# Kernel tuning notes

Measured on AMD Instinct MI355X. Metric: run time of the kernel, lower is better.

## Reference

```python
import jax, jax.numpy as jnp
import numpy as np

B, S, E = 8, 2048, 512
H = 8          # attention heads (and also number of sampling points)
P = 8          # deformable sampling points per token
Dh = E // H


def setup_inputs() -> dict:
    key = jax.random.key(0)
    ks = jax.random.split(key, 9)
    scale = 0.02
    return {
        "q": jax.random.normal(ks[0], (B, S, E), jnp.float32),
        "k": jax.random.normal(ks[1], (B, S, E), jnp.float32),
        "v": jax.random.normal(ks[2], (B, S, E), jnp.float32),
        "offset_w": jax.random.normal(ks[3], (2 * P, E), jnp.float32) * scale,
        "offset_b": jnp.zeros((2 * P,), jnp.float32),
        "in_proj_w": jax.random.normal(ks[4], (3 * E, E), jnp.float32) * scale,
        "in_proj_b": jnp.zeros((3 * E,), jnp.float32),
        "out_w": jax.random.normal(ks[5], (E, E), jnp.float32) * scale,
        "out_b": jnp.zeros((E,), jnp.float32),
    }


def reference(q, k, v, offset_w, offset_b, in_proj_w, in_proj_b, out_w, out_b):
    b, s, e = q.shape
    # learned offsets: [B,S,P,2]; only component 0 is used as a temporal offset
    offsets = (q @ offset_w.T + offset_b).reshape(b, s, P, 2)
    t = jnp.arange(s, dtype=q.dtype)[None, :, None]                # [1,S,1]
    # index = clamp(int(t + off0), 0, S-1); python int() truncates toward zero
    idx = jnp.clip(jnp.trunc(t + offsets[..., 0]).astype(jnp.int32), 0, s - 1)  # [B,S,P]
    # gather sampled K/V: [B,S,P,E]
    sk = jnp.take_along_axis(k[:, :, None, :], idx[..., None], axis=1)
    sv = jnp.take_along_axis(v[:, :, None, :], idx[..., None], axis=1)

    # nn.MultiheadAttention with query len 1 per token, kv len P, batch = B*S
    wq, wk, wv = in_proj_w[:e], in_proj_w[e:2 * e], in_proj_w[2 * e:]
    bq, bk, bv = in_proj_b[:e], in_proj_b[e:2 * e], in_proj_b[2 * e:]
    n = b * s
    qp = (q.reshape(n, e) @ wq.T + bq).reshape(n, H, Dh)            # [N,H,Dh]
    kp = (sk.reshape(n, P, e) @ wk.T + bk).reshape(n, P, H, Dh)     # [N,P,H,Dh]
    vp = (sv.reshape(n, P, e) @ wv.T + bv).reshape(n, P, H, Dh)
    scores = jnp.einsum('nhd,nphd->nhp', qp, kp) / np.sqrt(Dh)      # [N,H,P]
    attn = jax.nn.softmax(scores, axis=-1)
    ctx = jnp.einsum('nhp,nphd->nhd', attn, vp).reshape(n, e)       # [N,E]
    out = ctx @ out_w.T + out_b
    return out.reshape(b, s, e)
```

## Files before the change

kernel.cpp:

```cpp
#include <hip/hip_runtime.h>

#define S_LEN 2048
#define E_DIM 512
#define NTOK  16384

typedef __bf16 bf16x8_t __attribute__((ext_vector_type(8)));
typedef float f32x4_t __attribute__((ext_vector_type(4)));
typedef unsigned short u16x8_t __attribute__((ext_vector_type(8)));

__device__ __forceinline__ float bf2f(unsigned short h) {
  return __uint_as_float(((unsigned)h) << 16);
}
__device__ __forceinline__ u16x8_t cvt8n(float4 a, float4 b) {
  bf16x8_t t;
  t[0] = (__bf16)a.x; t[1] = (__bf16)a.y; t[2] = (__bf16)a.z; t[3] = (__bf16)a.w;
  t[4] = (__bf16)b.x; t[5] = (__bf16)b.y; t[6] = (__bf16)b.z; t[7] = (__bf16)b.w;
  union { bf16x8_t h; u16x8_t u; } cv; cv.h = t; return cv.u;
}
__device__ __forceinline__ void gload16(const void* g, void* l) {
  __builtin_amdgcn_global_load_lds(
      (const __attribute__((address_space(1))) unsigned int*)g,
      (__attribute__((address_space(3))) unsigned int*)l, 16, 0, 0);
}

__global__ __launch_bounds__(256)
void offsets_kernel(const float* __restrict__ q, const float* __restrict__ ow,
                    const float* __restrict__ ob, int* __restrict__ idx,
                    unsigned short* __restrict__ Qbf)
{
  const int wid  = threadIdx.x >> 6;
  const int lane = threadIdx.x & 63;
  const int n = blockIdx.x * 4 + wid;
  const int s = n & (S_LEN - 1);
  const float* qr = q + (size_t)n * E_DIM + lane * 8;
  const float4 q0 = *(const float4*)qr;
  const float4 q1 = *(const float4*)(qr + 4);
  *(u16x8_t*)(Qbf + (size_t)n * E_DIM + lane * 8) = cvt8n(q0, q1);
  float myoff = 0.f;
  #pragma unroll
  for (int p = 0; p < 8; ++p) {
    const float* wr = ow + (size_t)(2 * p) * E_DIM + lane * 8;
    const float4 w0 = *(const float4*)wr;
    const float4 w1 = *(const float4*)(wr + 4);
    float acc = q0.x*w0.x + q0.y*w0.y + q0.z*w0.z + q0.w*w0.w
              + q1.x*w1.x + q1.y*w1.y + q1.z*w1.z + q1.w*w1.w;
    #pragma unroll
    for (int d = 32; d; d >>= 1) acc += __shfl_xor(acc, d, 64);
    if ((lane & 7) == p) myoff = acc;
  }
  if (lane < 8) {
    float off = myoff + ob[2 * lane];
    float val = (float)s + off;
    int id = (int)truncf(val);
    id = id < 0 ? 0 : (id > S_LEN - 1 ? S_LEN - 1 : id);
    idx[n * 8 + lane] = id;
  }
}

__global__ __launch_bounds__(256)
void cvt_kernel(const float* __restrict__ k, const float* __restrict__ v,
                const float* __restrict__ ipw, const float* __restrict__ ow,
                unsigned short* __restrict__ Kb, unsigned short* __restrict__ Vb,
                unsigned short* __restrict__ Wb, unsigned short* __restrict__ OWb)
{
  const int bid = blockIdx.x;
  const float* src; unsigned short* dst; size_t off;
  if (bid < 4096)       { src = k;   dst = Kb;  off = (size_t)bid * 2048; }
  else if (bid < 8192)  { src = v;   dst = Vb;  off = (size_t)(bid - 4096) * 2048; }
  else if (bid < 8576)  { src = ipw; dst = Wb;  off = (size_t)(bid - 8192) * 2048; }
  else                  { src = ow;  dst = OWb; off = (size_t)(bid - 8576) * 2048; }
  const size_t i = off + (size_t)threadIdx.x * 8;
  const float4 a = *(const float4*)(src + i);
  const float4 b = *(const float4*)(src + i + 4);
  *(u16x8_t*)(dst + i) = cvt8n(a, b);
}

template<int OUT_BF16>
__global__ __launch_bounds__(256, 2)
void gemm_kernel(const unsigned short* __restrict__ A0, const unsigned short* __restrict__ A1,
                 const unsigned short* __restrict__ A2, const unsigned short* __restrict__ W,
                 const float* __restrict__ bias, void* __restrict__ Cout)
{
  __shared__ __align__(16) unsigned short sA[2][128 * 64];
  __shared__ __align__(16) unsigned short sB[2][128 * 64];

  const int z = blockIdx.z;
  const unsigned short* A = (z == 0) ? A0 : ((z == 1) ? A1 : A2);
  const unsigned short* Wz = W + (size_t)z * E_DIM * E_DIM;
  const float* bz = bias + (size_t)z * E_DIM;

  const int t    = threadIdx.x;
  const int lane = t & 63;
  const int wid  = t >> 6;
  const int wm   = wid >> 1;
  const int wn   = wid & 1;
  const size_t m0 = (size_t)blockIdx.x * 128;
  const size_t n0 = (size_t)blockIdx.y * 128;

  const int srow0  = wid * 32;
  const int schunk = (lane & 7) ^ (lane >> 3);
  const unsigned short* gA = A  + (m0 + srow0 + (lane >> 3)) * E_DIM + schunk * 8;
  const unsigned short* gB = Wz + (n0 + srow0 + (lane >> 3)) * E_DIM + schunk * 8;

#define STAGE(buf, k0) do { \
    _Pragma("unroll") \
    for (int i_ = 0; i_ < 4; ++i_) { \
      gload16(gA + (size_t)(i_ * 8) * E_DIM + (k0), &sA[buf][(srow0 + i_ * 8) * 64]); \
      gload16(gB + (size_t)(i_ * 8) * E_DIM + (k0), &sB[buf][(srow0 + i_ * 8) * 64]); \
    } } while (0)

  f32x4_t acc[4][4];
  #pragma unroll
  for (int i = 0; i < 4; ++i)
    #pragma unroll
    for (int j = 0; j < 4; ++j)
      acc[i][j] = (f32x4_t){0.f, 0.f, 0.f, 0.f};

  STAGE(0, 0);
  int cur = 0;
  const int fr = lane & 15;
  const int ck0 = lane >> 4;

  for (int kt = 0; kt < 8; ++kt) {
    __syncthreads();
    if (kt < 7) STAGE(cur ^ 1, (kt + 1) * 64);
    #pragma unroll
    for (int kk = 0; kk < 64; kk += 32) {
      const int ckb = (kk >> 3) + ck0;
      bf16x8_t af[4], bfv[4];
      #pragma unroll
      for (int i = 0; i < 4; ++i) {
        const int ra = wm * 64 + i * 16 + fr;
        af[i] = *(const bf16x8_t*)&sA[cur][ra * 64 + ((ckb ^ (ra & 7)) << 3)];
      }
      #pragma unroll
      for (int j = 0; j < 4; ++j) {
        const int rb = wn * 64 + j * 16 + fr;
        bfv[j] = *(const bf16x8_t*)&sB[cur][rb * 64 + ((ckb ^ (rb & 7)) << 3)];
      }
      #pragma unroll
      for (int i = 0; i < 4; ++i)
        #pragma unroll
        for (int j = 0; j < 4; ++j)
          acc[i][j] = __builtin_amdgcn_mfma_f32_16x16x32_bf16(af[i], bfv[j], acc[i][j], 0, 0, 0);
    }
    cur ^= 1;
  }
#undef STAGE

  unsigned short* Cb = (unsigned short*)Cout + (size_t)z * NTOK * E_DIM;
  float* Cf = (float*)Cout;
  #pragma unroll
  for (int i = 0; i < 4; ++i) {
    const int row = (int)m0 + wm * 64 + i * 16 + (lane >> 4) * 4;
    #pragma unroll
    for (int j = 0; j < 4; ++j) {
      const int col = (int)n0 + wn * 64 + j * 16 + fr;
      const float bv = bz[col];
      #pragma unroll
      for (int r = 0; r < 4; ++r) {
        const float val = acc[i][j][r] + bv;
        if constexpr (OUT_BF16)
          Cb[(size_t)(row + r) * E_DIM + col] = __builtin_bit_cast(unsigned short, (__bf16)val);
        else
          Cf[(size_t)(row + r) * E_DIM + col] = val;
      }
    }
  }
}

__global__ __launch_bounds__(256)
void attn_kernel(const unsigned short* __restrict__ Qp, const unsigned short* __restrict__ Kp,
                 const unsigned short* __restrict__ Vp, const int* __restrict__ idx,
                 unsigned short* __restrict__ ctx)
{
  const int wid  = threadIdx.x >> 6;
  const int lane = threadIdx.x & 63;
  const int n = blockIdx.x * 4 + wid;
  const int b = n >> 11;
  const int h = lane >> 3;
  const int p = lane & 7;

  const int id = idx[n * 8 + p];
  const size_t krow = ((size_t)(b << 11) + id) * E_DIM + h * 64;
  const unsigned short* qb = Qp + (size_t)n * E_DIM + h * 64;

  float sc = 0.f;
  #pragma unroll
  for (int j = 0; j < 8; ++j) {
    u16x8_t qv = *(const u16x8_t*)(qb + j * 8);
    u16x8_t kv = *(const u16x8_t*)(Kp + krow + j * 8);
    #pragma unroll
    for (int e = 0; e < 8; ++e) sc += bf2f(qv[e]) * bf2f(kv[e]);
  }
  sc *= 0.125f;

  float m = sc;
  m = fmaxf(m, __shfl_xor(m, 1, 64));
  m = fmaxf(m, __shfl_xor(m, 2, 64));
  m = fmaxf(m, __shfl_xor(m, 4, 64));
  const float ex = __expf(sc - m);
  float dsum = ex;
  dsum += __shfl_xor(dsum, 1, 64);
  dsum += __shfl_xor(dsum, 2, 64);
  dsum += __shfl_xor(dsum, 4, 64);
  const float attn = ex / dsum;

  const int d0 = p * 8;
  float cacc[8];
  #pragma unroll
  for (int j = 0; j < 8; ++j) cacc[j] = 0.f;
  #pragma unroll
  for (int pp = 0; pp < 8; ++pp) {
    const float ap = __shfl(attn, (lane & 56) + pp, 64);
    const int  idp = __shfl(id,   (lane & 56) + pp, 64);
    const unsigned short* vb = Vp + ((size_t)(b << 11) + idp) * E_DIM + h * 64 + d0;
    u16x8_t vv = *(const u16x8_t*)vb;
    #pragma unroll
    for (int j = 0; j < 8; ++j) cacc[j] += ap * bf2f(vv[j]);
  }
  u16x8_t cc;
  #pragma unroll
  for (int j = 0; j < 8; ++j) cc[j] = __builtin_bit_cast(unsigned short, (__bf16)cacc[j]);
  *(u16x8_t*)(ctx + (size_t)n * E_DIM + h * 64 + d0) = cc;
}

extern "C" void kernel_launch(void* const* d_in, const int* in_sizes, int n_in,
                              void* d_out, int out_size, void* d_ws, size_t ws_size,
                              hipStream_t stream) {
  const float* q        = (const float*)d_in[0];
  const float* k        = (const float*)d_in[1];
  const float* v        = (const float*)d_in[2];
  const float* offset_w = (const float*)d_in[3];
  const float* offset_b = (const float*)d_in[4];
  const float* in_proj_w = (const float*)d_in[5];
  const float* in_proj_b = (const float*)d_in[6];
  const float* out_w    = (const float*)d_in[7];
  const float* out_b    = (const float*)d_in[8];

  char* ws = (char*)d_ws;
  unsigned short* Qbf = (unsigned short*)ws;
  unsigned short* Kbf = Qbf + (size_t)NTOK * E_DIM;
  unsigned short* Vbf = Kbf + (size_t)NTOK * E_DIM;
  unsigned short* Wb  = Vbf + (size_t)NTOK * E_DIM;
  unsigned short* OWb = Wb + (size_t)3 * E_DIM * E_DIM;
  unsigned short* Qp  = OWb + (size_t)E_DIM * E_DIM;
  unsigned short* Kp  = Qp + (size_t)NTOK * E_DIM;
  unsigned short* Vp  = Kp + (size_t)NTOK * E_DIM;
  int* idxb = (int*)(Vp + (size_t)NTOK * E_DIM);
  unsigned short* ctxb = Qbf;

  offsets_kernel<<<NTOK / 4, 256, 0, stream>>>(q, offset_w, offset_b, idxb, Qbf);
  cvt_kernel<<<8704, 256, 0, stream>>>(k, v, in_proj_w, out_w, Kbf, Vbf, Wb, OWb);
  gemm_kernel<1><<<dim3(NTOK / 128, E_DIM / 128, 3), 256, 0, stream>>>(
      Qbf, Kbf, Vbf, Wb, in_proj_b, (void*)Qp);
  attn_kernel<<<NTOK / 4, 256, 0, stream>>>(Qp, Kp, Vp, idxb, ctxb);
  gemm_kernel<0><<<dim3(NTOK / 128, E_DIM / 128, 1), 256, 0, stream>>>(
      ctxb, ctxb, ctxb, OWb, out_b, d_out);
}
```

Before: 105.5 us.

## Merge prepass kernels and deepen GEMM pipeline to four-stage K=32 ring

Fuses the offsets and conversion kernels into one launch with block-range dispatch, which removes one kernel launch and its tail. The GEMM moves from a double-buffered K=64 tile to a four-slot ring of K=32 tiles. It uses explicit vmcnt waits, raw barriers and setprio around the MFMA block, so more global loads stay in flight. In exchange it adds two barriers per K-step, a new swizzle and hand-tuned waitcnt counts that could break if the compiler reorders loads.

```diff
diff --git a/kernel.cpp b/kernel.cpp
--- a/kernel.cpp
+++ b/kernel.cpp
@@ -24,13 +24,30 @@
 }
 
 __global__ __launch_bounds__(256)
-void offsets_kernel(const float* __restrict__ q, const float* __restrict__ ow,
+void prepass_kernel(const float* __restrict__ q, const float* __restrict__ k,
+                    const float* __restrict__ v, const float* __restrict__ ipw,
+                    const float* __restrict__ outw, const float* __restrict__ ow,
                     const float* __restrict__ ob, int* __restrict__ idx,
-                    unsigned short* __restrict__ Qbf)
+                    unsigned short* __restrict__ Qbf, unsigned short* __restrict__ Kb,
+                    unsigned short* __restrict__ Vb, unsigned short* __restrict__ Wb,
+                    unsigned short* __restrict__ OWb)
 {
+  const int bid = blockIdx.x;
+  if (bid >= 4096) {
+    const float* src; unsigned short* dst; size_t off;
+    if (bid < 8192)       { src = k;    dst = Kb;  off = (size_t)(bid - 4096) * 2048; }
+    else if (bid < 12288) { src = v;    dst = Vb;  off = (size_t)(bid - 8192) * 2048; }
+    else if (bid < 12672) { src = ipw;  dst = Wb;  off = (size_t)(bid - 12288) * 2048; }
+    else                  { src = outw; dst = OWb; off = (size_t)(bid - 12672) * 2048; }
+    const size_t i = off + (size_t)threadIdx.x * 8;
+    const float4 a = *(const float4*)(src + i);
+    const float4 b = *(const float4*)(src + i + 4);
+    *(u16x8_t*)(dst + i) = cvt8n(a, b);
+    return;
+  }
   const int wid  = threadIdx.x >> 6;
   const int lane = threadIdx.x & 63;
-  const int n = blockIdx.x * 4 + wid;
+  const int n = bid * 4 + wid;
   const int s = n & (S_LEN - 1);
   const float* qr = q + (size_t)n * E_DIM + lane * 8;
   const float4 q0 = *(const float4*)qr;
@@ -57,32 +74,14 @@
   }
 }
 
-__global__ __launch_bounds__(256)
-void cvt_kernel(const float* __restrict__ k, const float* __restrict__ v,
-                const float* __restrict__ ipw, const float* __restrict__ ow,
-                unsigned short* __restrict__ Kb, unsigned short* __restrict__ Vb,
-                unsigned short* __restrict__ Wb, unsigned short* __restrict__ OWb)
-{
-  const int bid = blockIdx.x;
-  const float* src; unsigned short* dst; size_t off;
-  if (bid < 4096)       { src = k;   dst = Kb;  off = (size_t)bid * 2048; }
-  else if (bid < 8192)  { src = v;   dst = Vb;  off = (size_t)(bid - 4096) * 2048; }
-  else if (bid < 8576)  { src = ipw; dst = Wb;  off = (size_t)(bid - 8192) * 2048; }
-  else                  { src = ow;  dst = OWb; off = (size_t)(bid - 8576) * 2048; }
-  const size_t i = off + (size_t)threadIdx.x * 8;
-  const float4 a = *(const float4*)(src + i);
-  const float4 b = *(const float4*)(src + i + 4);
-  *(u16x8_t*)(dst + i) = cvt8n(a, b);
-}
-
 template<int OUT_BF16>
 __global__ __launch_bounds__(256, 2)
 void gemm_kernel(const unsigned short* __restrict__ A0, const unsigned short* __restrict__ A1,
                  const unsigned short* __restrict__ A2, const unsigned short* __restrict__ W,
                  const float* __restrict__ bias, void* __restrict__ Cout)
 {
-  __shared__ __align__(16) unsigned short sA[2][128 * 64];
-  __shared__ __align__(16) unsigned short sB[2][128 * 64];
+  __shared__ __align__(16) unsigned short sA[4][128 * 32];
+  __shared__ __align__(16) unsigned short sB[4][128 * 32];
 
   const int z = blockIdx.z;
   const unsigned short* A = (z == 0) ? A0 : ((z == 1) ? A1 : A2);
@@ -97,17 +96,17 @@
   const size_t m0 = (size_t)blockIdx.x * 128;
   const size_t n0 = (size_t)blockIdx.y * 128;
 
-  const int srow0  = wid * 32;
-  const int schunk = (lane & 7) ^ (lane >> 3);
-  const unsigned short* gA = A  + (m0 + srow0 + (lane >> 3)) * E_DIM + schunk * 8;
-  const unsigned short* gB = Wz + (n0 + srow0 + (lane >> 3)) * E_DIM + schunk * 8;
-
-#define STAGE(buf, k0) do { \
-    _Pragma("unroll") \
-    for (int i_ = 0; i_ < 4; ++i_) { \
-      gload16(gA + (size_t)(i_ * 8) * E_DIM + (k0), &sA[buf][(srow0 + i_ * 8) * 64]); \
-      gload16(gB + (size_t)(i_ * 8) * E_DIM + (k0), &sB[buf][(srow0 + i_ * 8) * 64]); \
-    } } while (0)
+  const int srow   = wid * 32 + (lane >> 2);
+  const int schunk = (lane & 3) ^ ((lane >> 3) & 3);
+  const unsigned short* gA = A  + (m0 + srow) * E_DIM + schunk * 8;
+  const unsigned short* gB = Wz + (n0 + srow) * E_DIM + schunk * 8;
+
+#define STAGE(slot, t_) do { \
+    gload16(gA + (t_) * 32,              &sA[slot][(wid * 32) * 32]); \
+    gload16(gA + (t_) * 32 + 16 * E_DIM, &sA[slot][(wid * 32 + 16) * 32]); \
+    gload16(gB + (t_) * 32,              &sB[slot][(wid * 32) * 32]); \
+    gload16(gB + (t_) * 32 + 16 * E_DIM, &sB[slot][(wid * 32 + 16) * 32]); \
+  } while (0)
 
   f32x4_t acc[4][4];
   #pragma unroll
@@ -116,35 +115,39 @@
     for (int j = 0; j < 4; ++j)
       acc[i][j] = (f32x4_t){0.f, 0.f, 0.f, 0.f};
 
-  STAGE(0, 0);
-  int cur = 0;
-  const int fr = lane & 15;
-  const int ck0 = lane >> 4;
-
-  for (int kt = 0; kt < 8; ++kt) {
-    __syncthreads();
-    if (kt < 7) STAGE(cur ^ 1, (kt + 1) * 64);
-    #pragma unroll
-    for (int kk = 0; kk < 64; kk += 32) {
-      const int ckb = (kk >> 3) + ck0;
-      bf16x8_t af[4], bfv[4];
+  STAGE(0, 0); STAGE(1, 1); STAGE(2, 2);
+
+  const int fr    = lane & 15;
+  const int cswz8 = (((lane >> 4) ^ ((fr >> 1) & 3)) << 3);
+
+  #pragma unroll
+  for (int tt = 0; tt < 16; ++tt) {
+    if (tt + 3 < 16) STAGE((tt + 3) & 3, tt + 3);
+    if (tt < 13)       asm volatile("s_waitcnt vmcnt(12)" ::: "memory");
+    else if (tt == 13) asm volatile("s_waitcnt vmcnt(8)"  ::: "memory");
+    else if (tt == 14) asm volatile("s_waitcnt vmcnt(4)"  ::: "memory");
+    else               asm volatile("s_waitcnt vmcnt(0)"  ::: "memory");
+    __builtin_amdgcn_sched_barrier(0);
+    __builtin_amdgcn_s_barrier();
+    __builtin_amdgcn_sched_barrier(0);
+    const int sl = tt & 3;
+    bf16x8_t af[4], bfv[4];
+    #pragma unroll
+    for (int i = 0; i < 4; ++i)
+      af[i] = *(const bf16x8_t*)&sA[sl][(wm * 64 + i * 16 + fr) * 32 + cswz8];
+    #pragma unroll
+    for (int j = 0; j < 4; ++j)
+      bfv[j] = *(const bf16x8_t*)&sB[sl][(wn * 64 + j * 16 + fr) * 32 + cswz8];
+    __builtin_amdgcn_s_setprio(1);
+    #pragma unroll
+    for (int i = 0; i < 4; ++i)
       #pragma unroll
-      for (int i = 0; i < 4; ++i) {
-        const int ra = wm * 64 + i * 16 + fr;
-        af[i] = *(const bf16x8_t*)&sA[cur][ra * 64 + ((ckb ^ (ra & 7)) << 3)];
-      }
-      #pragma unroll
-      for (int j = 0; j < 4; ++j) {
-        const int rb = wn * 64 + j * 16 + fr;
-        bfv[j] = *(const bf16x8_t*)&sB[cur][rb * 64 + ((ckb ^ (rb & 7)) << 3)];
-      }
-      #pragma unroll
-      for (int i = 0; i < 4; ++i)
-        #pragma unroll
-        for (int j = 0; j < 4; ++j)
-          acc[i][j] = __builtin_amdgcn_mfma_f32_16x16x32_bf16(af[i], bfv[j], acc[i][j], 0, 0, 0);
-    }
-    cur ^= 1;
+      for (int j = 0; j < 4; ++j)
+        acc[i][j] = __builtin_amdgcn_mfma_f32_16x16x32_bf16(af[i], bfv[j], acc[i][j], 0, 0, 0);
+    __builtin_amdgcn_s_setprio(0);
+    __builtin_amdgcn_sched_barrier(0);
+    __builtin_amdgcn_s_barrier();
+    __builtin_amdgcn_sched_barrier(0);
   }
 #undef STAGE
 
@@ -250,8 +253,8 @@
   int* idxb = (int*)(Vp + (size_t)NTOK * E_DIM);
   unsigned short* ctxb = Qbf;
 
-  offsets_kernel<<<NTOK / 4, 256, 0, stream>>>(q, offset_w, offset_b, idxb, Qbf);
-  cvt_kernel<<<8704, 256, 0, stream>>>(k, v, in_proj_w, out_w, Kbf, Vbf, Wb, OWb);
+  prepass_kernel<<<12800, 256, 0, stream>>>(q, k, v, in_proj_w, out_w, offset_w, offset_b,
+                                            idxb, Qbf, Kbf, Vbf, Wb, OWb);
   gemm_kernel<1><<<dim3(NTOK / 128, E_DIM / 128, 3), 256, 0, stream>>>(
       Qbf, Kbf, Vbf, Wb, in_proj_b, (void*)Qp);
   attn_kernel<<<NTOK / 4, 256, 0, stream>>>(Qp, Kp, Vp, idxb, ctxb);
```

Result: slower. 109.4 us (+3.7%).

## Merge offset and conversion kernels into one prepass with LDS-staged offset dot products

Applied to the files above, without the earlier changes.

Combines the offsets kernel and the fp32-to-bf16 conversion kernel into a single launch, where the first 1024 blocks compute offsets and the rest convert K, V and the weights. The offset computation is restructured: the offset weights and each token's q row are staged in padded LDS, and each lane computes a partial dot product for one sampling point over a 64-element slice, followed by a three-step shuffle reduction instead of eight full-wave reductions. This removes one launch and its tail gap and cuts shuffle work. The cost is more LDS traffic, __syncthreads in the offset blocks, and more tokens handled per block.

```diff
diff --git a/kernel.cpp b/kernel.cpp
--- a/kernel.cpp
+++ b/kernel.cpp
@@ -3,6 +3,7 @@
 #define S_LEN 2048
 #define E_DIM 512
 #define NTOK  16384
+#define QBLK  1024
 
 typedef __bf16 bf16x8_t __attribute__((ext_vector_type(8)));
 typedef float f32x4_t __attribute__((ext_vector_type(4)));
@@ -24,55 +25,79 @@
 }
 
 __global__ __launch_bounds__(256)
-void offsets_kernel(const float* __restrict__ q, const float* __restrict__ ow,
+void prepass_kernel(const float* __restrict__ q, const float* __restrict__ k,
+                    const float* __restrict__ v, const float* __restrict__ ipw,
+                    const float* __restrict__ outw, const float* __restrict__ ow,
                     const float* __restrict__ ob, int* __restrict__ idx,
-                    unsigned short* __restrict__ Qbf)
-{
-  const int wid  = threadIdx.x >> 6;
-  const int lane = threadIdx.x & 63;
-  const int n = blockIdx.x * 4 + wid;
-  const int s = n & (S_LEN - 1);
-  const float* qr = q + (size_t)n * E_DIM + lane * 8;
-  const float4 q0 = *(const float4*)qr;
-  const float4 q1 = *(const float4*)(qr + 4);
-  *(u16x8_t*)(Qbf + (size_t)n * E_DIM + lane * 8) = cvt8n(q0, q1);
-  float myoff = 0.f;
-  #pragma unroll
-  for (int p = 0; p < 8; ++p) {
-    const float* wr = ow + (size_t)(2 * p) * E_DIM + lane * 8;
-    const float4 w0 = *(const float4*)wr;
-    const float4 w1 = *(const float4*)(wr + 4);
-    float acc = q0.x*w0.x + q0.y*w0.y + q0.z*w0.z + q0.w*w0.w
-              + q1.x*w1.x + q1.y*w1.y + q1.z*w1.z + q1.w*w1.w;
-    #pragma unroll
-    for (int d = 32; d; d >>= 1) acc += __shfl_xor(acc, d, 64);
-    if ((lane & 7) == p) myoff = acc;
-  }
-  if (lane < 8) {
-    float off = myoff + ob[2 * lane];
-    float val = (float)s + off;
-    int id = (int)truncf(val);
-    id = id < 0 ? 0 : (id > S_LEN - 1 ? S_LEN - 1 : id);
-    idx[n * 8 + lane] = id;
-  }
-}
-
-__global__ __launch_bounds__(256)
-void cvt_kernel(const float* __restrict__ k, const float* __restrict__ v,
-                const float* __restrict__ ipw, const float* __restrict__ ow,
-                unsigned short* __restrict__ Kb, unsigned short* __restrict__ Vb,
-                unsigned short* __restrict__ Wb, unsigned short* __restrict__ OWb)
+                    unsigned short* __restrict__ Qbf, unsigned short* __restrict__ Kb,
+                    unsigned short* __restrict__ Vb, unsigned short* __restrict__ Wb,
+                    unsigned short* __restrict__ OWb)
 {
   const int bid = blockIdx.x;
-  const float* src; unsigned short* dst; size_t off;
-  if (bid < 4096)       { src = k;   dst = Kb;  off = (size_t)bid * 2048; }
-  else if (bid < 8192)  { src = v;   dst = Vb;  off = (size_t)(bid - 4096) * 2048; }
-  else if (bid < 8576)  { src = ipw; dst = Wb;  off = (size_t)(bid - 8192) * 2048; }
-  else                  { src = ow;  dst = OWb; off = (size_t)(bid - 8576) * 2048; }
-  const size_t i = off + (size_t)threadIdx.x * 8;
-  const float4 a = *(const float4*)(src + i);
-  const float4 b = *(const float4*)(src + i + 4);
-  *(u16x8_t*)(dst + i) = cvt8n(a, b);
+  if (bid >= QBLK) {
+    const int cb = bid - QBLK;
+    const float* src; unsigned short* dst; size_t off;
+    if (cb < 4096)      { src = k;    dst = Kb;  off = (size_t)cb * 2048; }
+    else if (cb < 8192) { src = v;    dst = Vb;  off = (size_t)(cb - 4096) * 2048; }
+    else if (cb < 8576) { src = ipw;  dst = Wb;  off = (size_t)(cb - 8192) * 2048; }
+    else                { src = outw; dst = OWb; off = (size_t)(cb - 8576) * 2048; }
+    const size_t i = off + (size_t)threadIdx.x * 8;
+    const float4 a = *(const float4*)(src + i);
+    const float4 b = *(const float4*)(src + i + 4);
+    *(u16x8_t*)(dst + i) = cvt8n(a, b);
+    return;
+  }
+
+  __shared__ float wl[8][544];
+  __shared__ float ql[4][544];
+
+  {
+    const int r  = threadIdx.x >> 5;
+    const int e0 = (threadIdx.x & 31) * 16;
+    const float* src = ow + (size_t)(2 * r) * E_DIM + e0;
+    #pragma unroll
+    for (int c = 0; c < 4; ++c) {
+      const int e = e0 + c * 4;
+      *(float4*)&wl[r][(e >> 6) * 68 + (e & 63)] = *(const float4*)(src + c * 4);
+    }
+  }
+  __syncthreads();
+
+  const int w    = threadIdx.x >> 6;
+  const int lane = threadIdx.x & 63;
+  const int j    = lane >> 3;
+  const int p    = lane & 7;
+
+  for (int it = 0; it < 4; ++it) {
+    const int n = bid * 16 + w * 4 + it;
+    const float* qr = q + (size_t)n * E_DIM + lane * 8;
+    const float4 q0 = *(const float4*)qr;
+    const float4 q1 = *(const float4*)(qr + 4);
+    *(u16x8_t*)(Qbf + (size_t)n * E_DIM + lane * 8) = cvt8n(q0, q1);
+    const int e  = lane * 8;
+    const int ph = (e >> 6) * 68 + (e & 63);
+    *(float4*)&ql[w][ph]     = q0;
+    *(float4*)&ql[w][ph + 4] = q1;
+
+    float acc = 0.f;
+    #pragma unroll
+    for (int i4 = 0; i4 < 16; ++i4) {
+      const float4 qv = *(const float4*)&ql[w][j * 68 + i4 * 4];
+      const float4 wv = *(const float4*)&wl[p][j * 68 + i4 * 4];
+      acc = fmaf(qv.x, wv.x, acc); acc = fmaf(qv.y, wv.y, acc);
+      acc = fmaf(qv.z, wv.z, acc); acc = fmaf(qv.w, wv.w, acc);
+    }
+    acc += __shfl_xor(acc, 8, 64);
+    acc += __shfl_xor(acc, 16, 64);
+    acc += __shfl_xor(acc, 32, 64);
+    if (lane < 8) {
+      const float val = (float)(n & (S_LEN - 1)) + acc + ob[2 * lane];
+      int id = (int)truncf(val);
+      id = id < 0 ? 0 : (id > S_LEN - 1 ? S_LEN - 1 : id);
+      idx[n * 8 + lane] = id;
+    }
+    __syncthreads();
+  }
 }
 
 template<int OUT_BF16>
@@ -250,8 +275,8 @@
   int* idxb = (int*)(Vp + (size_t)NTOK * E_DIM);
   unsigned short* ctxb = Qbf;
 
-  offsets_kernel<<<NTOK / 4, 256, 0, stream>>>(q, offset_w, offset_b, idxb, Qbf);
-  cvt_kernel<<<8704, 256, 0, stream>>>(k, v, in_proj_w, out_w, Kbf, Vbf, Wb, OWb);
+  prepass_kernel<<<QBLK + 8704, 256, 0, stream>>>(q, k, v, in_proj_w, out_w, offset_w,
+                                                  offset_b, idxb, Qbf, Kbf, Vbf, Wb, OWb);
   gemm_kernel<1><<<dim3(NTOK / 128, E_DIM / 128, 3), 256, 0, stream>>>(
       Qbf, Kbf, Vbf, Wb, in_proj_b, (void*)Qp);
   attn_kernel<<<NTOK / 4, 256, 0, stream>>>(Qp, Kp, Vp, idxb, ctxb);
```

Measured after the change: 100.5 us. -4.7%, faster.

## Single-buffer GEMM LDS for higher occupancy and merge conversions into grid-stride kernel

Applied to the files above, without the earlier changes.

The GEMM drops double-buffered LDS staging in favour of a single buffer with two barriers per k-tile, and raises the launch-bounds occupancy hint from 2 to 4 blocks per CU. The aim is to hide latency through more resident waves instead of software prefetch. The q-to-bf16 conversion moves out of the offsets kernel into a single grid-stride conversion kernel that also handles k, v and the weights, using 4-wide conversion. The cost is that loads no longer overlap with MFMA inside a block, and offsets_kernel now reads q a second time.

```diff
diff --git a/kernel.cpp b/kernel.cpp
--- a/kernel.cpp
+++ b/kernel.cpp
@@ -3,10 +3,13 @@
 #define S_LEN 2048
 #define E_DIM 512
 #define NTOK  16384
+#define CVTBLK 4096
 
 typedef __bf16 bf16x8_t __attribute__((ext_vector_type(8)));
+typedef __bf16 bf16x4_t __attribute__((ext_vector_type(4)));
 typedef float f32x4_t __attribute__((ext_vector_type(4)));
 typedef unsigned short u16x8_t __attribute__((ext_vector_type(8)));
+typedef unsigned short u16x4_t __attribute__((ext_vector_type(4)));
 
 __device__ __forceinline__ float bf2f(unsigned short h) {
   return __uint_as_float(((unsigned)h) << 16);
@@ -17,6 +20,11 @@
   t[4] = (__bf16)b.x; t[5] = (__bf16)b.y; t[6] = (__bf16)b.z; t[7] = (__bf16)b.w;
   union { bf16x8_t h; u16x8_t u; } cv; cv.h = t; return cv.u;
 }
+__device__ __forceinline__ u16x4_t cvt4n(float4 a) {
+  bf16x4_t t;
+  t[0] = (__bf16)a.x; t[1] = (__bf16)a.y; t[2] = (__bf16)a.z; t[3] = (__bf16)a.w;
+  union { bf16x4_t h; u16x4_t u; } cv; cv.h = t; return cv.u;
+}
 __device__ __forceinline__ void gload16(const void* g, void* l) {
   __builtin_amdgcn_global_load_lds(
       (const __attribute__((address_space(1))) unsigned int*)g,
@@ -24,9 +32,29 @@
 }
 
 __global__ __launch_bounds__(256)
+void cvt_kernel(const float* __restrict__ q, const float* __restrict__ k,
+                const float* __restrict__ v, const float* __restrict__ ipw,
+                const float* __restrict__ outw,
+                unsigned short* __restrict__ Qbf, unsigned short* __restrict__ Kb,
+                unsigned short* __restrict__ Vb, unsigned short* __restrict__ Wb,
+                unsigned short* __restrict__ OWb)
+{
+  const size_t NG = 6553600;
+  const size_t gstride = (size_t)CVTBLK * 256;
+  for (size_t g = (size_t)blockIdx.x * 256 + threadIdx.x; g < NG; g += gstride) {
+    const float* src; unsigned short* dst; size_t e;
+    if (g < 2097152)      { src = q;    dst = Qbf; e = g * 4; }
+    else if (g < 4194304) { src = k;    dst = Kb;  e = (g - 2097152) * 4; }
+    else if (g < 6291456) { src = v;    dst = Vb;  e = (g - 4194304) * 4; }
+    else if (g < 6488064) { src = ipw;  dst = Wb;  e = (g - 6291456) * 4; }
+    else                  { src = outw; dst = OWb; e = (g - 6488064) * 4; }
+    *(u16x4_t*)(dst + e) = cvt4n(*(const float4*)(src + e));
+  }
+}
+
+__global__ __launch_bounds__(256)
 void offsets_kernel(const float* __restrict__ q, const float* __restrict__ ow,
-                    const float* __restrict__ ob, int* __restrict__ idx,
-                    unsigned short* __restrict__ Qbf)
+                    const float* __restrict__ ob, int* __restrict__ idx)
 {
   const int wid  = threadIdx.x >> 6;
   const int lane = threadIdx.x & 63;
@@ -35,7 +63,6 @@
   const float* qr = q + (size_t)n * E_DIM + lane * 8;
   const float4 q0 = *(const float4*)qr;
   const float4 q1 = *(const float4*)(qr + 4);
-  *(u16x8_t*)(Qbf + (size_t)n * E_DIM + lane * 8) = cvt8n(q0, q1);
   float myoff = 0.f;
   #pragma unroll
   for (int p = 0; p < 8; ++p) {
@@ -57,32 +84,14 @@
   }
 }
 
-__global__ __launch_bounds__(256)
-void cvt_kernel(const float* __restrict__ k, const float* __restrict__ v,
-                const float* __restrict__ ipw, const float* __restrict__ ow,
-                unsigned short* __restrict__ Kb, unsigned short* __restrict__ Vb,
-                unsigned short* __restrict__ Wb, unsigned short* __restrict__ OWb)
-{
-  const int bid = blockIdx.x;
-  const float* src; unsigned short* dst; size_t off;
-  if (bid < 4096)       { src = k;   dst = Kb;  off = (size_t)bid * 2048; }
-  else if (bid < 8192)  { src = v;   dst = Vb;  off = (size_t)(bid - 4096) * 2048; }
-  else if (bid < 8576)  { src = ipw; dst = Wb;  off = (size_t)(bid - 8192) * 2048; }
-  else                  { src = ow;  dst = OWb; off = (size_t)(bid - 8576) * 2048; }
-  const size_t i = off + (size_t)threadIdx.x * 8;
-  const float4 a = *(const float4*)(src + i);
-  const float4 b = *(const float4*)(src + i + 4);
-  *(u16x8_t*)(dst + i) = cvt8n(a, b);
-}
-
 template<int OUT_BF16>
-__global__ __launch_bounds__(256, 2)
+__global__ __launch_bounds__(256, 4)
 void gemm_kernel(const unsigned short* __restrict__ A0, const unsigned short* __restrict__ A1,
                  const unsigned short* __restrict__ A2, const unsigned short* __restrict__ W,
                  const float* __restrict__ bias, void* __restrict__ Cout)
 {
-  __shared__ __align__(16) unsigned short sA[2][128 * 64];
-  __shared__ __align__(16) unsigned short sB[2][128 * 64];
+  __shared__ __align__(16) unsigned short sA[128 * 64];
+  __shared__ __align__(16) unsigned short sB[128 * 64];
 
   const int z = blockIdx.z;
   const unsigned short* A = (z == 0) ? A0 : ((z == 1) ? A1 : A2);
@@ -102,11 +111,11 @@
   const unsigned short* gA = A  + (m0 + srow0 + (lane >> 3)) * E_DIM + schunk * 8;
   const unsigned short* gB = Wz + (n0 + srow0 + (lane >> 3)) * E_DIM + schunk * 8;
 
-#define STAGE(buf, k0) do { \
+#define STAGE(k0) do { \
     _Pragma("unroll") \
     for (int i_ = 0; i_ < 4; ++i_) { \
-      gload16(gA + (size_t)(i_ * 8) * E_DIM + (k0), &sA[buf][(srow0 + i_ * 8) * 64]); \
-      gload16(gB + (size_t)(i_ * 8) * E_DIM + (k0), &sB[buf][(srow0 + i_ * 8) * 64]); \
+      gload16(gA + (size_t)(i_ * 8) * E_DIM + (k0), &sA[(srow0 + i_ * 8) * 64]); \
+      gload16(gB + (size_t)(i_ * 8) * E_DIM + (k0), &sB[(srow0 + i_ * 8) * 64]); \
     } } while (0)
 
   f32x4_t acc[4][4];
@@ -116,14 +125,13 @@
     for (int j = 0; j < 4; ++j)
       acc[i][j] = (f32x4_t){0.f, 0.f, 0.f, 0.f};
 
-  STAGE(0, 0);
-  int cur = 0;
   const int fr = lane & 15;
   const int ck0 = lane >> 4;
 
   for (int kt = 0; kt < 8; ++kt) {
     __syncthreads();
-    if (kt < 7) STAGE(cur ^ 1, (kt + 1) * 64);
+    STAGE(kt * 64);
+    __syncthreads();
     #pragma unroll
     for (int kk = 0; kk < 64; kk += 32) {
       const int ckb = (kk >> 3) + ck0;
@@ -131,12 +139,12 @@
       #pragma unroll
       for (int i = 0; i < 4; ++i) {
         const int ra = wm * 64 + i * 16 + fr;
-        af[i] = *(const bf16x8_t*)&sA[cur][ra * 64 + ((ckb ^ (ra & 7)) << 3)];
+        af[i] = *(const bf16x8_t*)&sA[ra * 64 + ((ckb ^ (ra & 7)) << 3)];
       }
       #pragma unroll
       for (int j = 0; j < 4; ++j) {
         const int rb = wn * 64 + j * 16 + fr;
-        bfv[j] = *(const bf16x8_t*)&sB[cur][rb * 64 + ((ckb ^ (rb & 7)) << 3)];
+        bfv[j] = *(const bf16x8_t*)&sB[rb * 64 + ((ckb ^ (rb & 7)) << 3)];
       }
       #pragma unroll
       for (int i = 0; i < 4; ++i)
@@ -144,7 +152,6 @@
         for (int j = 0; j < 4; ++j)
           acc[i][j] = __builtin_amdgcn_mfma_f32_16x16x32_bf16(af[i], bfv[j], acc[i][j], 0, 0, 0);
     }
-    cur ^= 1;
   }
 #undef STAGE
 
@@ -250,8 +257,8 @@
   int* idxb = (int*)(Vp + (size_t)NTOK * E_DIM);
   unsigned short* ctxb = Qbf;
 
-  offsets_kernel<<<NTOK / 4, 256, 0, stream>>>(q, offset_w, offset_b, idxb, Qbf);
-  cvt_kernel<<<8704, 256, 0, stream>>>(k, v, in_proj_w, out_w, Kbf, Vbf, Wb, OWb);
+  cvt_kernel<<<CVTBLK, 256, 0, stream>>>(q, k, v, in_proj_w, out_w, Qbf, Kbf, Vbf, Wb, OWb);
+  offsets_kernel<<<NTOK / 4, 256, 0, stream>>>(q, offset_w, offset_b, idxb);
   gemm_kernel<1><<<dim3(NTOK / 128, E_DIM / 128, 3), 256, 0, stream>>>(
       Qbf, Kbf, Vbf, Wb, in_proj_b, (void*)Qp);
   attn_kernel<<<NTOK / 4, 256, 0, stream>>>(Qp, Kp, Vp, idxb, ctxb);
```

Result: slower. 110.9 us (+5.2%).
